# Performance work log

Measured on AMD Instinct MI355X. Metric: run time of the kernel, lower is better.

Reference implementation:

```python
import jax, jax.numpy as jnp
import numpy as np

D_EMBED = 512
N_HEAD = 8
N_LAYER = 12
B, S = 4, 1024


def setup_inputs() -> dict:
    key = jax.random.key(0)
    ks = jax.random.split(key, 8)
    std = 0.02
    x = jax.random.normal(ks[0], (B, S, D_EMBED), dtype=jnp.float32)
    e = jax.random.normal(ks[1], (B, S, D_EMBED), dtype=jnp.float32)
    p = jax.random.normal(ks[2], (S, D_EMBED), dtype=jnp.float32)
    W_q = std * jax.random.normal(ks[3], (N_HEAD, D_EMBED, D_EMBED), dtype=jnp.float32)
    W_k = std * jax.random.normal(ks[4], (N_HEAD, D_EMBED, D_EMBED), dtype=jnp.float32)
    W_v = std * jax.random.normal(ks[5], (N_HEAD, D_EMBED, D_EMBED), dtype=jnp.float32)
    # torch Linear weight: (out_features, in_features) = (E, H*E)
    W_o = (std / np.sqrt(2 * N_LAYER)) * jax.random.normal(ks[6], (D_EMBED, N_HEAD * D_EMBED), dtype=jnp.float32)
    gamma = std * jax.random.normal(ks[7], (1, N_HEAD, 1, 1), dtype=jnp.float32)
    return {"x": x, "e": e, "p": p, "W_q": W_q, "W_k": W_k, "W_v": W_v, "W_o": W_o, "gamma": gamma}


def reference(x, e, p, W_q, W_k, W_v, W_o, gamma):
    # use_ppe_attn=False path: Q,K,V all from x. Per-head full-dim projections.
    Q = jnp.einsum('bse,hef->bhsf', x, W_q)  # (B,H,S,E)
    K = jnp.einsum('bse,hef->bhsf', x, W_k)
    V = jnp.einsum('bse,hef->bhsf', x, W_v)
    # rbf kernel: exp(-gamma * ||q - k||_2^2), squared distance via expansion
    q2 = jnp.sum(Q * Q, axis=-1, keepdims=True)          # (B,H,S,1)
    k2 = jnp.sum(K * K, axis=-1, keepdims=True)          # (B,H,S,1)
    qk = jnp.einsum('bhse,bhte->bhst', Q, K)             # (B,H,S,S)
    d2 = jnp.maximum(q2 + jnp.swapaxes(k2, -2, -1) - 2.0 * qk, 0.0)
    attn = jnp.exp(-gamma * d2)                          # (B,H,S,S)
    out = jnp.einsum('bhst,bhte->bhse', attn, V)         # (B,H,S,E)
    out = jnp.transpose(out, (0, 2, 1, 3)).reshape(x.shape[0], x.shape[1], -1)  # (B,S,H*E)
    return out @ W_o.T                                   # (B,S,E)
```

## Files before the change

kernel.cpp:

```cpp
#include <hip/hip_runtime.h>
#include <cstdint>
#include <cstring>

typedef unsigned short ushort_t;
typedef __attribute__((ext_vector_type(8))) short short8;
typedef __attribute__((ext_vector_type(4))) float f32x4;
typedef __attribute__((ext_vector_type(4))) unsigned short us4;

constexpr int Hh = 8;
constexpr int Ss = 1024;
constexpr int Ee = 512;

__device__ __forceinline__ ushort_t f2bf(float f) {
    uint32_t u; __builtin_memcpy(&u, &f, 4);
    u += 0x7fffu + ((u >> 16) & 1u);
    return (ushort_t)(u >> 16);
}
__device__ __forceinline__ float bf2f(ushort_t h) {
    uint32_t u = ((uint32_t)h) << 16; float f; __builtin_memcpy(&f, &u, 4); return f;
}

__device__ __forceinline__ void gload_lds16(const ushort_t* g, void* lds) {
    __builtin_amdgcn_global_load_lds(
        (const __attribute__((address_space(1))) void*)g,
        (__attribute__((address_space(3))) void*)lds, 16, 0, 0);
}


__global__ void cvt_f32_bf16(const float4* __restrict__ in, us4* __restrict__ out, int n4) {
    int i = blockIdx.x * blockDim.x + threadIdx.x;
    if (i < n4) {
        float4 v = in[i];
        us4 o = { f2bf(v.x), f2bf(v.y), f2bf(v.z), f2bf(v.w) };
        out[i] = o;
    }
}

__global__ void wtrans_all(const float* __restrict__ Wq, const float* __restrict__ Wk,
                           const float* __restrict__ Wv, ushort_t* __restrict__ Wt) {
    __shared__ float tile[32][33];
    int zz = blockIdx.z;
    int h = zz & 7, sel = zz >> 3;
    const float* W = (sel == 0 ? Wq : (sel == 1 ? Wk : Wv));
    int e0 = blockIdx.y * 32, f0 = blockIdx.x * 32;
    int tx = threadIdx.x, ty = threadIdx.y;
    #pragma unroll
    for (int i = 0; i < 4; i++) {
        int e = e0 + ty + i * 8;
        tile[ty + i * 8][tx] = W[((size_t)h * 512 + e) * 512 + f0 + tx];
    }
    __syncthreads();
    #pragma unroll
    for (int i = 0; i < 4; i++) {
        int f = f0 + ty + i * 8;
        Wt[((size_t)zz * 512 + f) * 512 + e0 + tx] = f2bf(tile[tx][ty + i * 8]);
    }
}

__global__ void sumsq(const ushort_t* __restrict__ X, float* __restrict__ out) {
    int row = blockIdx.x * 4 + (threadIdx.x >> 6);
    int ln = threadIdx.x & 63;
    short8 v = *(const short8*)(X + (size_t)row * 512 + ln * 8);
    float s = 0.f;
    #pragma unroll
    for (int j = 0; j < 8; j++) {
        float f = bf2f((ushort_t)v[j]);
        s += f * f;
    }
    #pragma unroll
    for (int off = 32; off > 0; off >>= 1) s += __shfl_xor(s, off);
    if (ln == 0) out[row] = s;
}

__global__ void reduce2(const f32x4* __restrict__ p, f32x4* __restrict__ out, int n4) {
    int i = blockIdx.x * blockDim.x + threadIdx.x;
    if (i < n4) out[i] = p[i] + p[i + (size_t)n4];
}

template<int EPI>
__device__ __forceinline__
void gemm256_body(const ushort_t* __restrict__ A, int lda,
                  const ushort_t* __restrict__ Bm, int ldb,
                  void* __restrict__ Cout, int K,
                  const float* __restrict__ q2, const float* __restrict__ k2,
                  const float* __restrict__ gamma, int bIdx,
                  void* __restrict__ Cout2)
{
    __shared__ __align__(16) ushort_t SMEM[65536];

    const int t  = threadIdx.x;
    const int wv = t >> 6, ln = t & 63;
    const int wm = wv >> 2, wn = wv & 3;

    const int gx = gridDim.x, gy = gridDim.y;
    const int gxy = gx * gy;
    const int L = blockIdx.x + gx * (blockIdx.y + gy * blockIdx.z);
    const int xcd = L & 7;
    const int j = L >> 3;
    const int z  = xcd + 8 * (j / gxy);
    const int rem = j % gxy;
    const int by = rem / gx;
    const int bx = rem % gx;

    const int m0 = by * 256, n0 = bx * 256;

    int bh = z;
    if constexpr (EPI == 2 || EPI == 3) bh = (bIdx < 0) ? z : (bIdx * Hh + z);

    const ushort_t* Ab = A;
    const ushort_t* Bb = Bm;
    if constexpr (EPI == 5) { Bb = Bm + (size_t)z * Ee * Ee; }
    if constexpr (EPI == 2) {
        Ab = A  + (size_t)bh * Ss * Ee;
        Bb = Bm + (size_t)bh * Ss * Ee;
    }
    if constexpr (EPI == 3) {
        Ab = A  + (size_t)z * Ss * Ss;
        Bb = Bm + (size_t)bh * Ee * Ss;
    }

    f32x4 acc[8][4];
    #pragma unroll
    for (int i = 0; i < 8; i++)
        #pragma unroll
        for (int j2 = 0; j2 < 4; j2++) acc[i][j2] = (f32x4){0.f, 0.f, 0.f, 0.f};

    const int srow = ln >> 3;
    const int schk = ((ln & 7) ^ srow) * 8;
    const ushort_t* sbase[4][2];
    int ldso[4][2];
    #pragma unroll
    for (int kind = 0; kind < 4; ++kind) {
        #pragma unroll
        for (int c = 0; c < 2; ++c) {
            const int idx = (kind & 1) * 16 + wv * 2 + c;
            const int rb = idx * 8 + srow;
            sbase[kind][c] = (kind < 2)
                ? Ab + (size_t)(m0 + rb) * lda + schk
                : Bb + (size_t)(n0 + rb) * ldb + schk;
            ldso[kind][c] = (kind < 2 ? 0 : 32768) + idx * 512;
        }
    }
    auto STAGE_UNIT = [&](int tile, int kind) {
        const int k0 = tile << 6;
        const int par = (tile & 1) * 16384;
        #pragma unroll
        for (int c = 0; c < 2; ++c)
            gload_lds16(sbase[kind][c] + k0, &SMEM[ldso[kind][c] + par]);
    };

    const int T = K >> 6;

    #pragma unroll
    for (int kk = 0; kk < 4; ++kk) STAGE_UNIT(0, kk);
    #pragma unroll
    for (int kk = 0; kk < 4; ++kk) STAGE_UNIT(1, kk);
    asm volatile("s_waitcnt vmcnt(8)" ::: "memory");
    __builtin_amdgcn_s_barrier();

    const int lrow = ln & 15, lkg = ln >> 4;
    const int swz = lrow & 7;

    for (int u = 0; u < (T >> 1); ++u) {
        short8 bfr[4][2];
        #pragma unroll
        for (int p = 0; p < 8; ++p) {
            const int d = p >> 2, q = p & 3;

            if (q == 0) {
                #pragma unroll
                for (int fc = 0; fc < 4; fc++)
                    #pragma unroll
                    for (int kg = 0; kg < 2; kg++)
                        bfr[fc][kg] = *(const short8*)(&SMEM[32768 + d * 16384 +
                                          (wn * 64 + fc * 16 + lrow) * 64 +
                                          (((kg * 4 + lkg) ^ swz) << 3)]);
            }
            short8 af[2][2];
            #pragma unroll
            for (int j2 = 0; j2 < 2; j2++)
                #pragma unroll
                for (int kg = 0; kg < 2; kg++)
                    af[j2][kg] = *(const short8*)(&SMEM[d * 16384 +
                                     (wm * 128 + (q * 2 + j2) * 16 + lrow) * 64 +
                                     (((kg * 4 + lkg) ^ swz) << 3)]);

            {
                int stile, skind;
                if      (p == 0) { stile = 2 * u + 1; skind = 0; }
                else if (p == 1) { stile = 2 * u + 1; skind = 1; }
                else if (p == 2) { stile = 2 * u + 2; skind = 2; }
                else if (p == 3) { stile = 2 * u + 2; skind = 3; }
                else if (p == 4) { stile = 2 * u + 2; skind = 0; }
                else if (p == 5) { stile = 2 * u + 2; skind = 1; }
                else if (p == 6) { stile = 2 * u + 3; skind = 2; }
                else             { stile = 2 * u + 3; skind = 3; }
                if (stile < T && !(u == 0 && stile == 1))
                    STAGE_UNIT(stile, skind);
            }

            __builtin_amdgcn_s_barrier();

            __builtin_amdgcn_s_setprio(1);
            #pragma unroll
            for (int j2 = 0; j2 < 2; j2++)
                #pragma unroll
                for (int fc = 0; fc < 4; fc++)
                    #pragma unroll
                    for (int kg = 0; kg < 2; kg++)
                        acc[q * 2 + j2][fc] = __builtin_amdgcn_mfma_f32_16x16x32_bf16(
                            af[j2][kg], bfr[fc][kg], acc[q * 2 + j2][fc], 0, 0, 0);
            __builtin_amdgcn_s_setprio(0);

            if (p == 3) {
                if (2 * u + 2 < T) asm volatile("s_waitcnt vmcnt(4)" ::: "memory");
                else               asm volatile("s_waitcnt vmcnt(0)" ::: "memory");
            }
            if (p == 7 && (u + 1) < (T >> 1)) {
                asm volatile("s_waitcnt vmcnt(4)" ::: "memory");
            }

            __builtin_amdgcn_s_barrier();
        }
    }

    const int crow = (ln >> 4) * 4, ccol = ln & 15;

    bool vtpath = false;
    if constexpr (EPI == 5) vtpath = ((z >> 3) == 2);

    if (vtpath) {
        ushort_t* O = (ushort_t*)Cout2;
        const int h = z & 7;
        #pragma unroll
        for (int fr = 0; fr < 8; fr++) {
            #pragma unroll
            for (int fc = 0; fc < 4; fc++) {
                int gm0 = m0 + wm * 128 + fr * 16 + crow;
                int gn  = n0 + wn * 64 + fc * 16 + ccol;
                int b = gm0 >> 10, s = gm0 & 1023;
                us4 pk = { f2bf(acc[fr][fc][0]), f2bf(acc[fr][fc][1]),
                           f2bf(acc[fr][fc][2]), f2bf(acc[fr][fc][3]) };
                *(us4*)(O + ((size_t)(b * Hh + h) * Ee + gn) * Ss + s) = pk;
            }
        }
    } else {
        ushort_t* scr = SMEM + wv * 4608;
        float g = 0.f; const float* q2b = nullptr; const float* k2b = nullptr;
        float k2v[4];
        if constexpr (EPI == 2) {
            g = gamma[z & 7];
            q2b = q2 + (size_t)bh * Ss;
            k2b = k2 + (size_t)bh * Ss;
            #pragma unroll
            for (int fc = 0; fc < 4; fc++) k2v[fc] = k2b[n0 + wn * 64 + fc * 16 + ccol];
        }
        for (int pass = 0; pass < 2; ++pass) {
            float q2p[4][4];
            if constexpr (EPI == 2) {
                #pragma unroll
                for (int fr2 = 0; fr2 < 4; fr2++)
                    #pragma unroll
                    for (int i = 0; i < 4; i++)
                        q2p[fr2][i] = q2b[m0 + wm * 128 + pass * 64 + fr2 * 16 + crow + i];
            }
            #pragma unroll
            for (int fr2 = 0; fr2 < 4; fr2++) {
                int fr = pass * 4 + fr2;
                #pragma unroll
                for (int fc = 0; fc < 4; fc++) {
                    #pragma unroll
                    for (int i = 0; i < 4; i++) {
                        float v = acc[fr][fc][i];
                        if constexpr (EPI == 2) {
                            float d2 = fmaxf(q2p[fr2][i] + k2v[fc] - 2.0f * v, 0.0f);
                            v = __expf(-g * d2);
                        }
                        scr[(fr2 * 16 + crow + i) * 72 + fc * 16 + ccol] = f2bf(v);
                    }
                }
            }
            #pragma unroll
            for (int rr = 0; rr < 8; ++rr) {
                int r = rr * 8 + (ln >> 3);
                int c = (ln & 7) * 8;
                short8 v = *(const short8*)&scr[r * 72 + c];
                int gm = m0 + wm * 128 + pass * 64 + r;
                int gn = n0 + wn * 64 + c;
                ushort_t* O = (ushort_t*)Cout;
                size_t addr;
                if constexpr (EPI == 5) {
                    int mat = z >> 3, h = z & 7;
                    int b = gm >> 10, s = gm & 1023;
                    addr = (size_t)mat * 16777216 + ((size_t)(b * Hh + h) * Ss + s) * Ee + gn;
                } else if constexpr (EPI == 2) {
                    addr = ((size_t)z * Ss + gm) * Ss + gn;
                } else {
                    int bo = (bIdx < 0) ? (z >> 3) : bIdx;
                    int hh = (bIdx < 0) ? (z & 7) : z;
                    addr = ((size_t)(bo * Ss + gm)) * (Hh * Ee) + (size_t)hh * Ee + gn;
                }
                *(short8*)&O[addr] = v;
            }
        }
    }
}

__global__ __launch_bounds__(512, 1)
void g_proj(const ushort_t* A, int lda, const ushort_t* Bm, int ldb, void* C, int K,
            const float* q2, const float* k2, const float* gamma, int bIdx, void* C2)
{ gemm256_body<5>(A, lda, Bm, ldb, C, K, q2, k2, gamma, bIdx, C2); }

__global__ __launch_bounds__(512, 1)
void g_scores(const ushort_t* A, int lda, const ushort_t* Bm, int ldb, void* C, int K,
              const float* q2, const float* k2, const float* gamma, int bIdx, void* C2)
{ gemm256_body<2>(A, lda, Bm, ldb, C, K, q2, k2, gamma, bIdx, C2); }

__global__ __launch_bounds__(512, 1)
void g_pv(const ushort_t* A, int lda, const ushort_t* Bm, int ldb, void* C, int K,
          const float* q2, const float* k2, const float* gamma, int bIdx, void* C2)
{ gemm256_body<3>(A, lda, Bm, ldb, C, K, q2, k2, gamma, bIdx, C2); }

__global__ __launch_bounds__(256)
void g_final(const ushort_t* __restrict__ A, int lda,
             const ushort_t* __restrict__ Bm, int ldb,
             float* __restrict__ Cout, int K)
{
    __shared__ __align__(16) ushort_t SMEM[16384];

    const int t  = threadIdx.x;
    const int wv = t >> 6, ln = t & 63;
    const int wr = wv >> 1, wc = wv & 1;

    const int gx = gridDim.x, gy = gridDim.y;
    const int nwg = gx * gy * gridDim.z;
    const int L = blockIdx.x + gx * (blockIdx.y + gy * blockIdx.z);
    const int wid = (L & 7) * (nwg >> 3) + (L >> 3);
    const int bx = wid % gx;
    const int tmp = wid / gx;
    const int by = tmp % gy;
    const int z  = tmp / gy;

    const int m0 = by * 128, n0 = bx * 128;
    const ushort_t* Ab = A  + (size_t)z * 2048;
    const ushort_t* Bb = Bm + (size_t)z * 2048;

    f32x4 acc[4][4];
    #pragma unroll
    for (int i = 0; i < 4; i++)
        #pragma unroll
        for (int j = 0; j < 4; j++) acc[i][j] = (f32x4){0.f, 0.f, 0.f, 0.f};

    const int rstage = t >> 2;
    const int cchunk = t & 3;

    auto STAGE = [&](int ti, int buf) {
        const int k0 = ti << 5;
        #pragma unroll
        for (int i = 0; i < 2; i++) {
            gload_lds16(Ab + (size_t)(m0 + i * 64 + rstage) * lda + k0 + cchunk * 8,
                        (char*)SMEM + buf * 8192 + i * 4096 + wv * 1024);
            gload_lds16(Bb + (size_t)(n0 + i * 64 + rstage) * ldb + k0 + cchunk * 8,
                        (char*)SMEM + 16384 + buf * 8192 + i * 4096 + wv * 1024);
        }
    };

    const int nt = K >> 5;
    STAGE(0, 0);
    __syncthreads();

    int cur = 0;
    const int lrow = ln & 15, kg = ln >> 4;
    for (int ti = 0; ti < nt; ++ti) {
        if (ti + 1 < nt) STAGE(ti + 1, cur ^ 1);

        short8 af[4], bfr[4];
        #pragma unroll
        for (int fr = 0; fr < 4; fr++)
            af[fr] = *(const short8*)(&SMEM[cur * 4096 + (wr * 64 + fr * 16 + lrow) * 32 + kg * 8]);
        #pragma unroll
        for (int fc = 0; fc < 4; fc++)
            bfr[fc] = *(const short8*)(&SMEM[8192 + cur * 4096 + (wc * 64 + fc * 16 + lrow) * 32 + kg * 8]);
        #pragma unroll
        for (int fr = 0; fr < 4; fr++)
            #pragma unroll
            for (int fc = 0; fc < 4; fc++)
                acc[fr][fc] = __builtin_amdgcn_mfma_f32_16x16x32_bf16(af[fr], bfr[fc], acc[fr][fc], 0, 0, 0);

        __syncthreads();
        cur ^= 1;
    }

    const int crow = (ln >> 4) * 4, ccol = ln & 15;
    float* O = Cout + (size_t)z * 4096 * 512;
    float* fscr = (float*)SMEM + wv * 1088;
    #pragma unroll
    for (int pass = 0; pass < 4; ++pass) {
        #pragma unroll
        for (int fc = 0; fc < 4; fc++)
            #pragma unroll
            for (int i = 0; i < 4; i++)
                fscr[(crow + i) * 68 + fc * 16 + ccol] = acc[pass][fc][i];
        #pragma unroll
        for (int rr = 0; rr < 4; ++rr) {
            int r = rr * 4 + (ln >> 4);
            int c = (ln & 15) * 4;
            f32x4 v = *(const f32x4*)&fscr[r * 68 + c];
            int gm = m0 + wr * 64 + pass * 16 + r;
            int gn = n0 + wc * 64 + c;
            *(f32x4*)&O[(size_t)gm * 512 + gn] = v;
        }
    }
}


extern "C" void kernel_launch(void* const* d_in, const int* in_sizes, int n_in,
                              void* d_out, int out_size, void* d_ws, size_t ws_size,
                              hipStream_t stream)
{
    const float* x     = (const float*)d_in[0];
    const float* Wq    = (const float*)d_in[3];
    const float* Wk    = (const float*)d_in[4];
    const float* Wv    = (const float*)d_in[5];
    const float* Wo    = (const float*)d_in[6];
    const float* gamma = (const float*)d_in[7];

    char* ws = (char*)d_ws;
    size_t off = 0;
    auto alloc = [&](size_t bytes) -> void* {
        void* p = ws + off;
        off += (bytes + 255) & ~(size_t)255;
        return p;
    };
    ushort_t* xb    = (ushort_t*)alloc(4096ull * 512 * 2);
    ushort_t* Wt    = (ushort_t*)alloc(24ull * 512 * 512 * 2);
    ushort_t* WoB   = (ushort_t*)alloc(512ull * 4096 * 2);
    ushort_t* Qb    = (ushort_t*)alloc(4ull * 8 * 1024 * 512 * 2);
    ushort_t* Kb    = (ushort_t*)alloc(4ull * 8 * 1024 * 512 * 2);
    ushort_t* Vt    = (ushort_t*)alloc(4ull * 8 * 512 * 1024 * 2);
    float*    q2    = (float*)alloc(32768ull * 4);
    float*    k2    = (float*)alloc(32768ull * 4);

    size_t off_common = off;
    size_t need_merged = off_common + 64ull * 1024 * 1024;
    bool merged = (ws_size >= need_merged);

    ushort_t* attn;
    ushort_t* Ob;
    float* fpart;
    if (merged) {
        attn = (ushort_t*)alloc(32ull * 1024 * 1024 * 2);
        Ob   = Qb;
        fpart = (float*)attn;
    } else {
        attn = (ushort_t*)alloc(8ull * 1024 * 1024 * 2);
        Ob   = (ushort_t*)alloc(4096ull * 4096 * 2);
        fpart = (float*)Qb;
    }
    (void)in_sizes; (void)n_in; (void)out_size;

    cvt_f32_bf16<<<2048, 256, 0, stream>>>((const float4*)x,  (us4*)xb,  524288);
    cvt_f32_bf16<<<2048, 256, 0, stream>>>((const float4*)Wo, (us4*)WoB, 524288);

    dim3 tb(32, 8);
    wtrans_all<<<dim3(16, 16, 24), tb, 0, stream>>>(Wq, Wk, Wv, Wt);

    g_proj<<<dim3(2, 16, 24), 512, 0, stream>>>(xb, 512, Wt, 512, Qb, 512,
                                                nullptr, nullptr, nullptr, 0, Vt);

    sumsq<<<16384, 256, 0, stream>>>(Qb, q2);

    if (merged) {
        g_scores<<<dim3(4, 4, 32), 512, 0, stream>>>(Qb, 512, Kb, 512, attn, 512, q2, k2, gamma, -1, nullptr);
        g_pv<<<dim3(2, 4, 32), 512, 0, stream>>>(attn, 1024, Vt, 1024, Ob, 1024, nullptr, nullptr, nullptr, -1, nullptr);
    } else {
        for (int b = 0; b < 4; b++) {
            g_scores<<<dim3(4, 4, 8), 512, 0, stream>>>(Qb, 512, Kb, 512, attn, 512, q2, k2, gamma, b, nullptr);
            g_pv<<<dim3(2, 4, 8), 512, 0, stream>>>(attn, 1024, Vt, 1024, Ob, 1024, nullptr, nullptr, nullptr, b, nullptr);
        }
    }

    g_final<<<dim3(4, 32, 2), 256, 0, stream>>>(Ob, 4096, WoB, 4096, fpart, 2048);
    reduce2<<<2048, 256, 0, stream>>>((const f32x4*)fpart, (f32x4*)d_out, 524288);
}
```

Baseline: 213.5 us.

## Fuse RBF score and PV GEMMs into a flash-style attention kernel

Replaces the separate scores GEMM (writing a bf16 B·H·S·S attention matrix to global memory) and the PV GEMM with a single fused kernel. Each workgroup holds a 64-row Q tile in registers, streams 32-key K and V tiles through double-buffered LDS, computes the RBF exp on the fly and accumulates P·V directly. This removes the large attention-matrix write and read and one launch. The cost is smaller 64x32 tiles with more barriers per step, lower MFMA density, and re-reading K/V once per query tile. The workspace-size branch is removed and the projection GEMM is de-templated.

```diff
diff --git a/kernel.cpp b/kernel.cpp
--- a/kernel.cpp
+++ b/kernel.cpp
@@ -77,14 +77,11 @@
     if (i < n4) out[i] = p[i] + p[i + (size_t)n4];
 }
 
-template<int EPI>
-__device__ __forceinline__
-void gemm256_body(const ushort_t* __restrict__ A, int lda,
-                  const ushort_t* __restrict__ Bm, int ldb,
-                  void* __restrict__ Cout, int K,
-                  const float* __restrict__ q2, const float* __restrict__ k2,
-                  const float* __restrict__ gamma, int bIdx,
-                  void* __restrict__ Cout2)
+__global__ __launch_bounds__(512, 1)
+void g_proj(const ushort_t* __restrict__ A, int lda,
+            const ushort_t* __restrict__ Bm, int ldb,
+            void* __restrict__ Cout, int K,
+            void* __restrict__ Cout2)
 {
     __shared__ __align__(16) ushort_t SMEM[65536];
 
@@ -104,20 +101,8 @@
 
     const int m0 = by * 256, n0 = bx * 256;
 
-    int bh = z;
-    if constexpr (EPI == 2 || EPI == 3) bh = (bIdx < 0) ? z : (bIdx * Hh + z);
-
     const ushort_t* Ab = A;
-    const ushort_t* Bb = Bm;
-    if constexpr (EPI == 5) { Bb = Bm + (size_t)z * Ee * Ee; }
-    if constexpr (EPI == 2) {
-        Ab = A  + (size_t)bh * Ss * Ee;
-        Bb = Bm + (size_t)bh * Ss * Ee;
-    }
-    if constexpr (EPI == 3) {
-        Ab = A  + (size_t)z * Ss * Ss;
-        Bb = Bm + (size_t)bh * Ee * Ss;
-    }
+    const ushort_t* Bb = Bm + (size_t)z * Ee * Ee;
 
     f32x4 acc[8][4];
     #pragma unroll
@@ -226,10 +211,7 @@
 
     const int crow = (ln >> 4) * 4, ccol = ln & 15;
 
-    bool vtpath = false;
-    if constexpr (EPI == 5) vtpath = ((z >> 3) == 2);
-
-    if (vtpath) {
+    if ((z >> 3) == 2) {
         ushort_t* O = (ushort_t*)Cout2;
         const int h = z & 7;
         #pragma unroll
@@ -246,39 +228,15 @@
         }
     } else {
         ushort_t* scr = SMEM + wv * 4608;
-        float g = 0.f; const float* q2b = nullptr; const float* k2b = nullptr;
-        float k2v[4];
-        if constexpr (EPI == 2) {
-            g = gamma[z & 7];
-            q2b = q2 + (size_t)bh * Ss;
-            k2b = k2 + (size_t)bh * Ss;
-            #pragma unroll
-            for (int fc = 0; fc < 4; fc++) k2v[fc] = k2b[n0 + wn * 64 + fc * 16 + ccol];
-        }
         for (int pass = 0; pass < 2; ++pass) {
-            float q2p[4][4];
-            if constexpr (EPI == 2) {
-                #pragma unroll
-                for (int fr2 = 0; fr2 < 4; fr2++)
-                    #pragma unroll
-                    for (int i = 0; i < 4; i++)
-                        q2p[fr2][i] = q2b[m0 + wm * 128 + pass * 64 + fr2 * 16 + crow + i];
-            }
             #pragma unroll
             for (int fr2 = 0; fr2 < 4; fr2++) {
                 int fr = pass * 4 + fr2;
                 #pragma unroll
-                for (int fc = 0; fc < 4; fc++) {
+                for (int fc = 0; fc < 4; fc++)
                     #pragma unroll
-                    for (int i = 0; i < 4; i++) {
-                        float v = acc[fr][fc][i];
-                        if constexpr (EPI == 2) {
-                            float d2 = fmaxf(q2p[fr2][i] + k2v[fc] - 2.0f * v, 0.0f);
-                            v = __expf(-g * d2);
-                        }
-                        scr[(fr2 * 16 + crow + i) * 72 + fc * 16 + ccol] = f2bf(v);
-                    }
-                }
+                    for (int i = 0; i < 4; i++)
+                        scr[(fr2 * 16 + crow + i) * 72 + fc * 16 + ccol] = f2bf(acc[fr][fc][i]);
             }
             #pragma unroll
             for (int rr = 0; rr < 8; ++rr) {
@@ -288,18 +246,9 @@
                 int gm = m0 + wm * 128 + pass * 64 + r;
                 int gn = n0 + wn * 64 + c;
                 ushort_t* O = (ushort_t*)Cout;
-                size_t addr;
-                if constexpr (EPI == 5) {
-                    int mat = z >> 3, h = z & 7;
-                    int b = gm >> 10, s = gm & 1023;
-                    addr = (size_t)mat * 16777216 + ((size_t)(b * Hh + h) * Ss + s) * Ee + gn;
-                } else if constexpr (EPI == 2) {
-                    addr = ((size_t)z * Ss + gm) * Ss + gn;
-                } else {
-                    int bo = (bIdx < 0) ? (z >> 3) : bIdx;
-                    int hh = (bIdx < 0) ? (z & 7) : z;
-                    addr = ((size_t)(bo * Ss + gm)) * (Hh * Ee) + (size_t)hh * Ee + gn;
-                }
+                int mat = z >> 3, h = z & 7;
+                int b = gm >> 10, s = gm & 1023;
+                size_t addr = (size_t)mat * 16777216 + ((size_t)(b * Hh + h) * Ss + s) * Ee + gn;
                 *(short8*)&O[addr] = v;
             }
         }
@@ -307,19 +256,136 @@
 }
 
 __global__ __launch_bounds__(512, 1)
-void g_proj(const ushort_t* A, int lda, const ushort_t* Bm, int ldb, void* C, int K,
-            const float* q2, const float* k2, const float* gamma, int bIdx, void* C2)
-{ gemm256_body<5>(A, lda, Bm, ldb, C, K, q2, k2, gamma, bIdx, C2); }
-
-__global__ __launch_bounds__(512, 1)
-void g_scores(const ushort_t* A, int lda, const ushort_t* Bm, int ldb, void* C, int K,
-              const float* q2, const float* k2, const float* gamma, int bIdx, void* C2)
-{ gemm256_body<2>(A, lda, Bm, ldb, C, K, q2, k2, gamma, bIdx, C2); }
-
-__global__ __launch_bounds__(512, 1)
-void g_pv(const ushort_t* A, int lda, const ushort_t* Bm, int ldb, void* C, int K,
-          const float* q2, const float* k2, const float* gamma, int bIdx, void* C2)
-{ gemm256_body<3>(A, lda, Bm, ldb, C, K, q2, k2, gamma, bIdx, C2); }
+void g_fused(const ushort_t* __restrict__ Qb, const ushort_t* __restrict__ Kb,
+             const ushort_t* __restrict__ Vt, ushort_t* __restrict__ Ob,
+             const float* __restrict__ q2, const float* __restrict__ k2,
+             const float* __restrict__ gamma)
+{
+    __shared__ __align__(16) ushort_t SMEM[67584];
+
+    const int t  = threadIdx.x;
+    const int wv = t >> 6, ln = t & 63;
+    const int lrow = ln & 15, lkg = ln >> 4;
+    const int crow = lkg * 4, ccol = lrow;
+
+    const int L = blockIdx.x + gridDim.x * blockIdx.y;
+    const int xcd = L & 7;
+    const int j = L >> 3;
+    const int bh = xcd + 8 * (j >> 4);
+    const int qx = j & 15;
+    const int q0 = qx * 64;
+    const int b = bh >> 3, h = bh & 7;
+
+    const int wq = wv >> 1, wkv = wv & 1;
+    const int wm2 = wv >> 2, wn2 = wv & 3;
+
+    const ushort_t* Qrow = Qb + ((size_t)bh * Ss + q0 + wq * 16 + lrow) * Ee + lkg * 8;
+    short8 qf[16];
+    #pragma unroll
+    for (int ks = 0; ks < 16; ks++) qf[ks] = *(const short8*)(Qrow + ks * 32);
+
+    const float g = gamma[h];
+    float q2v[4];
+    #pragma unroll
+    for (int i = 0; i < 4; i++) q2v[i] = q2[(size_t)bh * Ss + q0 + wq * 16 + crow + i];
+    const float* k2b = k2 + (size_t)bh * Ss;
+
+    const ushort_t* Kbase = Kb + (size_t)bh * Ss * Ee;
+    const ushort_t* Vbase = Vt + (size_t)bh * Ee * Ss;
+
+    auto STAGE_K = [&](int t0, int buf) {
+        #pragma unroll
+        for (int c = 0; c < 4; c++) {
+            int r = wv * 4 + c;
+            gload_lds16(Kbase + (size_t)(t0 + r) * Ee + ((ln ^ (r & 7)) * 8),
+                        &SMEM[buf * 16384 + r * 512 + ln * 8]);
+        }
+    };
+    auto STAGE_V = [&](int t0, int buf) {
+        #pragma unroll
+        for (int c = 0; c < 4; c++) {
+            int idx = wv * 4 + c;
+            int e = idx * 16 + (ln >> 2);
+            gload_lds16(Vbase + (size_t)e * Ss + t0 + (((ln & 3) ^ (e & 3)) * 8),
+                        &SMEM[32768 + buf * 16384 + idx * 512 + ln * 8]);
+        }
+    };
+
+    f32x4 oacc[2][8];
+    #pragma unroll
+    for (int mi = 0; mi < 2; mi++)
+        #pragma unroll
+        for (int fe = 0; fe < 8; fe++) oacc[mi][fe] = (f32x4){0.f, 0.f, 0.f, 0.f};
+
+    STAGE_K(0, 0); STAGE_V(0, 0);
+    __syncthreads();
+
+    int cur = 0;
+    for (int kt = 0; kt < 32; ++kt) {
+        if (kt + 1 < 32) { STAGE_K((kt + 1) * 32, cur ^ 1); STAGE_V((kt + 1) * 32, cur ^ 1); }
+
+        f32x4 s = (f32x4){0.f, 0.f, 0.f, 0.f};
+        const int kr = wkv * 16 + lrow;
+        #pragma unroll
+        for (int ks = 0; ks < 16; ks++) {
+            int c = ks * 4 + lkg;
+            short8 bf = *(const short8*)(&SMEM[cur * 16384 + kr * 512 + ((c ^ (kr & 7)) * 8)]);
+            s = __builtin_amdgcn_mfma_f32_16x16x32_bf16(qf[ks], bf, s, 0, 0, 0);
+        }
+
+        float k2c = k2b[kt * 32 + wkv * 16 + ccol];
+        #pragma unroll
+        for (int i = 0; i < 4; i++) {
+            float d2 = fmaxf(q2v[i] + k2c - 2.0f * s[i], 0.0f);
+            float pv = __expf(-g * d2);
+            int pr = wq * 16 + crow + i;
+            int pc = wkv * 16 + ccol;
+            int chunk = pc >> 3;
+            SMEM[65536 + pr * 32 + ((chunk ^ (pr & 3)) * 8) + (pc & 7)] = f2bf(pv);
+        }
+
+        asm volatile("s_waitcnt lgkmcnt(0)" ::: "memory");
+        __builtin_amdgcn_s_barrier();
+        __builtin_amdgcn_sched_barrier(0);
+
+        short8 vb[8];
+        #pragma unroll
+        for (int fe = 0; fe < 8; fe++) {
+            int er = wn2 * 128 + fe * 16 + lrow;
+            vb[fe] = *(const short8*)(&SMEM[32768 + cur * 16384 + er * 32 + ((lkg ^ (er & 3)) * 8)]);
+        }
+        #pragma unroll
+        for (int mi = 0; mi < 2; mi++) {
+            int pr = wm2 * 32 + mi * 16 + lrow;
+            short8 pa = *(const short8*)(&SMEM[65536 + pr * 32 + ((lkg ^ (pr & 3)) * 8)]);
+            #pragma unroll
+            for (int fe = 0; fe < 8; fe++)
+                oacc[mi][fe] = __builtin_amdgcn_mfma_f32_16x16x32_bf16(pa, vb[fe], oacc[mi][fe], 0, 0, 0);
+        }
+
+        asm volatile("s_waitcnt vmcnt(0)" ::: "memory");
+        __builtin_amdgcn_s_barrier();
+        __builtin_amdgcn_sched_barrier(0);
+        cur ^= 1;
+    }
+
+    ushort_t* scr = SMEM + wv * 4352;
+    #pragma unroll
+    for (int mi = 0; mi < 2; mi++)
+        #pragma unroll
+        for (int fe = 0; fe < 8; fe++)
+            #pragma unroll
+            for (int i = 0; i < 4; i++)
+                scr[(mi * 16 + crow + i) * 136 + fe * 16 + ccol] = f2bf(oacc[mi][fe][i]);
+    #pragma unroll
+    for (int rr = 0; rr < 8; rr++) {
+        int r = rr * 4 + lkg;
+        int c = lrow * 8;
+        short8 v = *(const short8*)&scr[r * 136 + c];
+        size_t addr = ((size_t)(b * Ss + q0 + wm2 * 32 + r)) * (Hh * Ee) + (size_t)h * Ee + wn2 * 128 + c;
+        *(short8*)&Ob[addr] = v;
+    }
+}
 
 __global__ __launch_bounds__(256)
 void g_final(const ushort_t* __restrict__ A, int lda,
@@ -440,24 +506,9 @@
     ushort_t* Vt    = (ushort_t*)alloc(4ull * 8 * 512 * 1024 * 2);
     float*    q2    = (float*)alloc(32768ull * 4);
     float*    k2    = (float*)alloc(32768ull * 4);
-
-    size_t off_common = off;
-    size_t need_merged = off_common + 64ull * 1024 * 1024;
-    bool merged = (ws_size >= need_merged);
-
-    ushort_t* attn;
-    ushort_t* Ob;
-    float* fpart;
-    if (merged) {
-        attn = (ushort_t*)alloc(32ull * 1024 * 1024 * 2);
-        Ob   = Qb;
-        fpart = (float*)attn;
-    } else {
-        attn = (ushort_t*)alloc(8ull * 1024 * 1024 * 2);
-        Ob   = (ushort_t*)alloc(4096ull * 4096 * 2);
-        fpart = (float*)Qb;
-    }
-    (void)in_sizes; (void)n_in; (void)out_size;
+    ushort_t* Ob    = (ushort_t*)alloc(4096ull * 4096 * 2);
+    float*    fpart = (float*)Qb;
+    (void)in_sizes; (void)n_in; (void)out_size; (void)ws_size;
 
     cvt_f32_bf16<<<2048, 256, 0, stream>>>((const float4*)x,  (us4*)xb,  524288);
     cvt_f32_bf16<<<2048, 256, 0, stream>>>((const float4*)Wo, (us4*)WoB, 524288);
@@ -465,20 +516,11 @@
     dim3 tb(32, 8);
     wtrans_all<<<dim3(16, 16, 24), tb, 0, stream>>>(Wq, Wk, Wv, Wt);
 
-    g_proj<<<dim3(2, 16, 24), 512, 0, stream>>>(xb, 512, Wt, 512, Qb, 512,
-                                                nullptr, nullptr, nullptr, 0, Vt);
+    g_proj<<<dim3(2, 16, 24), 512, 0, stream>>>(xb, 512, Wt, 512, Qb, 512, Vt);
 
     sumsq<<<16384, 256, 0, stream>>>(Qb, q2);
 
-    if (merged) {
-        g_scores<<<dim3(4, 4, 32), 512, 0, stream>>>(Qb, 512, Kb, 512, attn, 512, q2, k2, gamma, -1, nullptr);
-        g_pv<<<dim3(2, 4, 32), 512, 0, stream>>>(attn, 1024, Vt, 1024, Ob, 1024, nullptr, nullptr, nullptr, -1, nullptr);
-    } else {
-        for (int b = 0; b < 4; b++) {
-            g_scores<<<dim3(4, 4, 8), 512, 0, stream>>>(Qb, 512, Kb, 512, attn, 512, q2, k2, gamma, b, nullptr);
-            g_pv<<<dim3(2, 4, 8), 512, 0, stream>>>(attn, 1024, Vt, 1024, Ob, 1024, nullptr, nullptr, nullptr, b, nullptr);
-        }
-    }
+    g_fused<<<dim3(16, 32), 512, 0, stream>>>(Qb, Kb, Vt, Ob, q2, k2, gamma);
 
     g_final<<<dim3(4, 32, 2), 256, 0, stream>>>(Ob, 4096, WoB, 4096, fpart, 2048);
     reduce2<<<2048, 256, 0, stream>>>((const f32x4*)fpart, (f32x4*)d_out, 524288);
```

Measured after the change: 258.4 us. +21.0%, slower.
